# Kernel optimization log

Hardware: AMD Instinct MI355X
Metric: run time of the kernel (lower is better)

Reference implementation:

```python
import jax, jax.numpy as jnp
import numpy as np

N_NODES = 100000
N_EDGES = 1600000
N_FEAT = 64
HIDDEN = 64
N_GRAPHS = 256


def setup_inputs() -> dict:
    key = jax.random.key(0)
    ks = jax.random.split(key, 8)
    x = jax.random.normal(ks[0], (N_NODES, N_FEAT), dtype=jnp.float32)
    edge_index = jax.random.randint(ks[1], (2, N_EDGES), 0, N_NODES, dtype=jnp.int64)
    batch = jnp.sort(jax.random.randint(ks[2], (N_NODES,), 0, N_GRAPHS, dtype=jnp.int64))
    W1 = jax.random.normal(ks[3], (N_FEAT, HIDDEN), dtype=jnp.float32) / np.sqrt(N_FEAT)
    b1 = jnp.zeros((HIDDEN,), dtype=jnp.float32)
    W2 = jax.random.normal(ks[4], (HIDDEN, HIDDEN), dtype=jnp.float32) / np.sqrt(HIDDEN)
    b2 = jnp.zeros((HIDDEN,), dtype=jnp.float32)
    Wfc = jax.random.normal(ks[5], (HIDDEN, 1), dtype=jnp.float32) / np.sqrt(HIDDEN)
    bfc = jnp.zeros((1,), dtype=jnp.float32)
    return {"x": x, "edge_index": edge_index, "batch": batch,
            "W1": W1, "b1": b1, "W2": W2, "b2": b2, "Wfc": Wfc, "bfc": bfc}


def _gcn_conv(x, W, b, src, dst, norm, n_nodes):
    # h = X W, then symmetric-normalized scatter-add aggregation at dst
    h = x @ W  # [N, H]
    msg = h[src] * norm[:, None]  # [E+N, H] gather + scale
    agg = jax.ops.segment_sum(msg, dst, num_segments=n_nodes)
    return agg + b


def reference(x, edge_index, batch, W1, b1, W2, b2, Wfc, bfc):
    n = x.shape[0]
    loops = jnp.arange(n, dtype=edge_index.dtype)
    src = jnp.concatenate([edge_index[0], loops])  # add self-loops (GCNConv default)
    dst = jnp.concatenate([edge_index[1], loops])
    deg = jax.ops.segment_sum(jnp.ones_like(dst, dtype=x.dtype), dst, num_segments=n)
    dinv = jnp.where(deg > 0, jax.lax.rsqrt(deg), 0.0)
    norm = dinv[src] * dinv[dst]  # D^-1/2 (A+I) D^-1/2

    h = jax.nn.relu(_gcn_conv(x, W1, b1, src, dst, norm, n))  # dropout = identity (eval)
    h = jax.nn.relu(_gcn_conv(h, W2, b2, src, dst, norm, n))

    # global mean pool over graphs
    sums = jax.ops.segment_sum(h, batch, num_segments=N_GRAPHS)
    counts = jax.ops.segment_sum(jnp.ones((n,), dtype=h.dtype), batch, num_segments=N_GRAPHS)
    pooled = sums / jnp.maximum(counts, 1.0)[:, None]  # [G, H]
    return jax.nn.sigmoid(pooled @ Wfc + bfc)  # [G, 1]
```

## Files before the change

kernel.cpp:

```cpp
#include <hip/hip_runtime.h>
#include <hip/hip_fp16.h>
#include <math.h>

#define N_NODES  100000
#define N_EDGES  1600000
#define NF       64
#define N_GRAPHS 256

#define BSH   7
#define NB    ((N_NODES + 127) / 128)
#define BCAP  2600

typedef float f32x2 __attribute__((ext_vector_type(2)));

__global__ void k_zerocur(int* __restrict__ bucketCur, float* __restrict__ gsum,
                          int* __restrict__ Ah8, int* __restrict__ Ah8b) {
    int i = blockIdx.x * blockDim.x + threadIdx.x;
    if (i < NB) bucketCur[i] = 0;
    if (i < N_GRAPHS) gsum[i] = 0.0f;
    if (i < 16) {
        Ah8 [(size_t)N_NODES * 16 + i] = 0;
        Ah8b[(size_t)N_NODES * 16 + i] = 0;
    }
}

__global__ __launch_bounds__(1024) void k_bscatter(const int* __restrict__ src,
                                                   const int* __restrict__ dst,
                                                   int* __restrict__ bucketCur,
                                                   int* __restrict__ scratch) {
    __shared__ int hist[NB];
    __shared__ int bbase[NB];
    int t = threadIdx.x;
    for (int i = t; i < NB; i += 1024) hist[i] = 0;
    __syncthreads();
    int e0 = (blockIdx.x * 1024 + t) * 8;
    int d[8], s[8], r[8];
    bool act = (e0 + 7) < N_EDGES;
    if (act) {
        *(int4*)&d[0] = *(const int4*)(dst + e0);
        *(int4*)&d[4] = *(const int4*)(dst + e0 + 4);
        *(int4*)&s[0] = *(const int4*)(src + e0);
        *(int4*)&s[4] = *(const int4*)(src + e0 + 4);
#pragma unroll
        for (int k = 0; k < 8; ++k) r[k] = atomicAdd(&hist[d[k] >> BSH], 1);
    }
    __syncthreads();
    for (int i = t; i < NB; i += 1024)
        if (hist[i]) bbase[i] = atomicAdd(&bucketCur[i], hist[i]);
    __syncthreads();
    if (act) {
#pragma unroll
        for (int k = 0; k < 8; ++k) {
            int b = d[k] >> BSH;
            int pos = bbase[b] + r[k];
            if (pos < BCAP)
                scratch[b * BCAP + pos] = ((d[k] & 127) << 17) | s[k];
        }
    }
}

__global__ __launch_bounds__(1024) void k_bscan(const int* __restrict__ bucketCur,
                                                int* __restrict__ bucketPtr,
                                                int* __restrict__ rowptr) {
    int t = threadIdx.x;
    __shared__ int ps[1024];
    int v = (t < NB) ? min(bucketCur[t], BCAP) : 0;
    ps[t] = v;
    __syncthreads();
#pragma unroll
    for (int off = 1; off < 1024; off <<= 1) {
        int u = (t >= off) ? ps[t - off] : 0;
        __syncthreads();
        ps[t] += u;
        __syncthreads();
    }
    if (t < NB) bucketPtr[t] = ps[t] - v;
    if (t == NB - 1) {
        bucketPtr[NB] = ps[t];
        rowptr[N_NODES] = ps[t];
    }
}

__global__ __launch_bounds__(256) void k_bfinal(const int* __restrict__ bucketCur,
                                                const int* __restrict__ bucketPtr,
                                                const int* __restrict__ scratch,
                                                int* __restrict__ rowptr,
                                                float* __restrict__ dinv,
                                                int* __restrict__ col) {
    int b = blockIdx.x;
    int cnt  = min(bucketCur[b], BCAP);
    int base = bucketPtr[b];
    int node0 = b << BSH;
    __shared__ int hist[128];
    __shared__ int escan[128];
    __shared__ int ps[128];
    __shared__ int rnk[BCAP];
    int t = threadIdx.x;
    if (t < 128) hist[t] = 0;
    __syncthreads();
    const int* sp = scratch + b * BCAP;
    for (int j = t; j < cnt; j += 256)
        rnk[j] = atomicAdd(&hist[sp[j] >> 17], 1);
    __syncthreads();
    int hv = (t < 128) ? hist[t] : 0;
    if (t < 128) ps[t] = hv;
    __syncthreads();
#pragma unroll
    for (int off = 1; off < 128; off <<= 1) {
        int u = 0;
        if (t < 128 && t >= off) u = ps[t - off];
        __syncthreads();
        if (t < 128) ps[t] += u;
        __syncthreads();
    }
    if (t < 128) {
        int excl = ps[t] - hv;
        escan[t] = excl;
        int node = node0 + t;
        if (node < N_NODES) {
            rowptr[node] = base + excl;
            dinv[node] = rsqrtf((float)(hv + 1));
        }
    }
    __syncthreads();
    for (int j = t; j < cnt; j += 256) {
        int pk = sp[j];
        col[base + escan[pk >> 17] + rnk[j]] = pk & 0x1FFFF;
    }
}

__device__ __forceinline__ void agg8(const int* __restrict__ rowptr,
                                     const int* __restrict__ col,
                                     const int* __restrict__ Ah8,
                                     int n, int oct,
                                     f32x2& a0, f32x2& a1, f32x2& a2, f32x2& a3) {
    int nn  = (n < N_NODES) ? n : N_NODES;
    int beg = 0, cnt = 0;
    if (n < N_NODES) { beg = rowptr[n]; cnt = rowptr[n + 1] - beg; }
    const int* cp = col + beg;
    {
        int2 raw = *(const int2*)(Ah8 + (size_t)nn * 16 + oct * 2);
        a0 += __builtin_amdgcn_cvt_pk_f32_fp8(raw.x, false);
        a1 += __builtin_amdgcn_cvt_pk_f32_fp8(raw.x, true);
        a2 += __builtin_amdgcn_cvt_pk_f32_fp8(raw.y, false);
        a3 += __builtin_amdgcn_cvt_pk_f32_fp8(raw.y, true);
    }
    int c[8];
#pragma unroll
    for (int p = 0; p < 8; ++p) {
        int v = cp[p];
        c[p] = (p < cnt) ? v : N_NODES;
    }
    for (int base = 0; base < cnt; base += 8) {
        int2 rr[8];
#pragma unroll
        for (int p = 0; p < 8; ++p)
            rr[p] = *(const int2*)(Ah8 + (size_t)c[p] * 16 + oct * 2);
        int nb = base + 8;
#pragma unroll
        for (int p = 0; p < 8; ++p) {
            int v = cp[nb + p];
            c[p] = (nb + p < cnt) ? v : N_NODES;
        }
#pragma unroll
        for (int p = 0; p < 8; ++p) {
            a0 += __builtin_amdgcn_cvt_pk_f32_fp8(rr[p].x, false);
            a1 += __builtin_amdgcn_cvt_pk_f32_fp8(rr[p].x, true);
            a2 += __builtin_amdgcn_cvt_pk_f32_fp8(rr[p].y, false);
            a3 += __builtin_amdgcn_cvt_pk_f32_fp8(rr[p].y, true);
        }
    }
}

__global__ __launch_bounds__(256) void k_gemm(const float* __restrict__ X,
                                              const float* __restrict__ W,
                                              const float* __restrict__ dinv,
                                              int* __restrict__ Ah8) {
    __shared__ float Ws[64][64];
    __shared__ float Xs[64][68];
    int t  = threadIdx.x;
    int n0 = blockIdx.x * 64;

    for (int i = t; i < 64 * 64; i += 256) Ws[i >> 6][i & 63] = W[i];

#pragma unroll
    for (int p = 0; p < 4; ++p) {
        int flat = p * 256 + t;
        int nl = flat >> 4;
        int kg = flat & 15;
        int node = n0 + nl;
        float4 v = make_float4(0.f, 0.f, 0.f, 0.f);
        if (node < N_NODES)
            v = *(const float4*)(X + (size_t)node * NF + kg * 4);
        Xs[kg * 4 + 0][nl] = v.x;
        Xs[kg * 4 + 1][nl] = v.y;
        Xs[kg * 4 + 2][nl] = v.z;
        Xs[kg * 4 + 3][nl] = v.w;
    }
    __syncthreads();

    int tx = t & 15;
    int ty = t >> 4;
    float acc[4][4];
#pragma unroll
    for (int i = 0; i < 4; ++i)
#pragma unroll
        for (int j = 0; j < 4; ++j) acc[i][j] = 0.f;

#pragma unroll 8
    for (int k = 0; k < 64; ++k) {
        float4 wv = *(const float4*)&Ws[k][tx * 4];
        float4 xv = *(const float4*)&Xs[k][ty * 4];
        acc[0][0] += xv.x * wv.x; acc[0][1] += xv.x * wv.y;
        acc[0][2] += xv.x * wv.z; acc[0][3] += xv.x * wv.w;
        acc[1][0] += xv.y * wv.x; acc[1][1] += xv.y * wv.y;
        acc[1][2] += xv.y * wv.z; acc[1][3] += xv.y * wv.w;
        acc[2][0] += xv.z * wv.x; acc[2][1] += xv.z * wv.y;
        acc[2][2] += xv.z * wv.z; acc[2][3] += xv.z * wv.w;
        acc[3][0] += xv.w * wv.x; acc[3][1] += xv.w * wv.y;
        acc[3][2] += xv.w * wv.z; acc[3][3] += xv.w * wv.w;
    }

#pragma unroll
    for (int i = 0; i < 4; ++i) {
        int node = n0 + ty * 4 + i;
        if (node < N_NODES) {
            float dv = dinv[node];
            int pk = 0;
            pk = __builtin_amdgcn_cvt_pk_fp8_f32(acc[i][0] * dv, acc[i][1] * dv, pk, false);
            pk = __builtin_amdgcn_cvt_pk_fp8_f32(acc[i][2] * dv, acc[i][3] * dv, pk, true);
            Ah8[(size_t)node * 16 + tx] = pk;
        }
    }
}

__global__ __launch_bounds__(256) void k_pullgemm(const int* __restrict__ rowptr,
                                                  const int* __restrict__ col,
                                                  const float* __restrict__ dinv,
                                                  const int* __restrict__ Ah8,
                                                  const float* __restrict__ W,
                                                  const float* __restrict__ bias,
                                                  int* __restrict__ AhOut) {
    __shared__ float Ws[64][64];
    __shared__ float Xs[64][68];
    int t  = threadIdx.x;
    int n0 = blockIdx.x * 64;

    for (int i = t; i < 64 * 64; i += 256) Ws[i >> 6][i & 63] = W[i];

    int wv      = t >> 6;
    int lane    = t & 63;
    int nodeSub = lane >> 3;
    int oct     = lane & 7;

    float4 bA = *(const float4*)(bias + oct * 8);
    float4 bB = *(const float4*)(bias + oct * 8 + 4);

#pragma unroll
    for (int r = 0; r < 2; ++r) {
        int nl = wv * 16 + r * 8 + nodeSub;
        int n  = n0 + nl;
        f32x2 a0 = {0.f, 0.f}, a1 = {0.f, 0.f}, a2 = {0.f, 0.f}, a3 = {0.f, 0.f};
        agg8(rowptr, col, Ah8, n, oct, a0, a1, a2, a3);
        float dv = (n < N_NODES) ? dinv[n] : 0.f;
        float f0 = a0.x * dv + bA.x; Xs[oct * 8 + 0][nl] = f0 > 0.f ? f0 : 0.f;
        float f1 = a0.y * dv + bA.y; Xs[oct * 8 + 1][nl] = f1 > 0.f ? f1 : 0.f;
        float f2 = a1.x * dv + bA.z; Xs[oct * 8 + 2][nl] = f2 > 0.f ? f2 : 0.f;
        float f3 = a1.y * dv + bA.w; Xs[oct * 8 + 3][nl] = f3 > 0.f ? f3 : 0.f;
        float f4 = a2.x * dv + bB.x; Xs[oct * 8 + 4][nl] = f4 > 0.f ? f4 : 0.f;
        float f5 = a2.y * dv + bB.y; Xs[oct * 8 + 5][nl] = f5 > 0.f ? f5 : 0.f;
        float f6 = a3.x * dv + bB.z; Xs[oct * 8 + 6][nl] = f6 > 0.f ? f6 : 0.f;
        float f7 = a3.y * dv + bB.w; Xs[oct * 8 + 7][nl] = f7 > 0.f ? f7 : 0.f;
    }
    __syncthreads();

    int tx = t & 15;
    int ty = t >> 4;
    float acc[4][4];
#pragma unroll
    for (int i = 0; i < 4; ++i)
#pragma unroll
        for (int j = 0; j < 4; ++j) acc[i][j] = 0.f;

#pragma unroll 8
    for (int k = 0; k < 64; ++k) {
        float4 wvv = *(const float4*)&Ws[k][tx * 4];
        float4 xv  = *(const float4*)&Xs[k][ty * 4];
        acc[0][0] += xv.x * wvv.x; acc[0][1] += xv.x * wvv.y;
        acc[0][2] += xv.x * wvv.z; acc[0][3] += xv.x * wvv.w;
        acc[1][0] += xv.y * wvv.x; acc[1][1] += xv.y * wvv.y;
        acc[1][2] += xv.y * wvv.z; acc[1][3] += xv.y * wvv.w;
        acc[2][0] += xv.z * wvv.x; acc[2][1] += xv.z * wvv.y;
        acc[2][2] += xv.z * wvv.z; acc[2][3] += xv.z * wvv.w;
        acc[3][0] += xv.w * wvv.x; acc[3][1] += xv.w * wvv.y;
        acc[3][2] += xv.w * wvv.z; acc[3][3] += xv.w * wvv.w;
    }

#pragma unroll
    for (int i = 0; i < 4; ++i) {
        int node = n0 + ty * 4 + i;
        if (node < N_NODES) {
            float dv = dinv[node];
            int pk = 0;
            pk = __builtin_amdgcn_cvt_pk_fp8_f32(acc[i][0] * dv, acc[i][1] * dv, pk, false);
            pk = __builtin_amdgcn_cvt_pk_fp8_f32(acc[i][2] * dv, acc[i][3] * dv, pk, true);
            AhOut[(size_t)node * 16 + tx] = pk;
        }
    }
}

__global__ __launch_bounds__(256) void k_pullpool(const int* __restrict__ rowptr,
                                                  const int* __restrict__ col,
                                                  const float* __restrict__ dinv,
                                                  const int* __restrict__ Ah8,
                                                  const float* __restrict__ b2,
                                                  const float* __restrict__ Wfc,
                                                  const int* __restrict__ batch,
                                                  float* __restrict__ gsum) {
    int t       = threadIdx.x;
    int lane    = t & 63;
    int wv      = t >> 6;
    int nodeSub = lane >> 3;
    int oct     = lane & 7;
    int n = blockIdx.x * 32 + wv * 8 + nodeSub;

    float4 bA = *(const float4*)(b2 + oct * 8);
    float4 bB = *(const float4*)(b2 + oct * 8 + 4);
    float4 wA = *(const float4*)(Wfc + oct * 8);
    float4 wB = *(const float4*)(Wfc + oct * 8 + 4);

    f32x2 a0 = {0.f, 0.f}, a1 = {0.f, 0.f}, a2 = {0.f, 0.f}, a3 = {0.f, 0.f};
    agg8(rowptr, col, Ah8, n, oct, a0, a1, a2, a3);

    int   g  = (n < N_NODES) ? (int)batch[n] : -1;
    float dv = (n < N_NODES) ? dinv[n] : 0.f;

    float wsum = 0.f;
    float v;
    v = a0.x * dv + bA.x; wsum += (v > 0.f ? v : 0.f) * wA.x;
    v = a0.y * dv + bA.y; wsum += (v > 0.f ? v : 0.f) * wA.y;
    v = a1.x * dv + bA.z; wsum += (v > 0.f ? v : 0.f) * wA.z;
    v = a1.y * dv + bA.w; wsum += (v > 0.f ? v : 0.f) * wA.w;
    v = a2.x * dv + bB.x; wsum += (v > 0.f ? v : 0.f) * wB.x;
    v = a2.y * dv + bB.y; wsum += (v > 0.f ? v : 0.f) * wB.y;
    v = a3.x * dv + bB.z; wsum += (v > 0.f ? v : 0.f) * wB.z;
    v = a3.y * dv + bB.w; wsum += (v > 0.f ? v : 0.f) * wB.w;
    wsum += __shfl_xor(wsum, 1);
    wsum += __shfl_xor(wsum, 2);
    wsum += __shfl_xor(wsum, 4);

    float sv = (oct == 0) ? wsum : 0.f;
    int   gv = (oct == 0) ? g : -2;
#pragma unroll
    for (int off = 8; off < 64; off <<= 1) {
        float s2 = __shfl_down(sv, off);
        int   g2 = __shfl_down(gv, off);
        if (g2 == gv) sv += s2;
    }
    int gp = __shfl_up(gv, 8);
    bool head = (lane < 8) || (gp != gv);
    if (oct == 0 && g >= 0 && head) atomicAdd(&gsum[g], sv);
}

__device__ __forceinline__ int lower_bound_i(const int* __restrict__ a, int n, int key) {
    int lo = 0, hi = n;
    while (lo < hi) {
        int mid = (lo + hi) >> 1;
        if (a[mid] < key) lo = mid + 1; else hi = mid;
    }
    return lo;
}

__global__ void k_final(const int* __restrict__ batch,
                        const float* __restrict__ gsum,
                        const float* __restrict__ bfc,
                        float* __restrict__ out) {
    int g = blockIdx.x * blockDim.x + threadIdx.x;
    if (g < N_GRAPHS) {
        int lo = lower_bound_i(batch, N_NODES, g);
        int hi = lower_bound_i(batch, N_NODES, g + 1);
        float c = (hi > lo) ? (float)(hi - lo) : 1.0f;
        float v = gsum[g] / c + bfc[0];
        out[g] = 1.0f / (1.0f + expf(-v));
    }
}

extern "C" void kernel_launch(void* const* d_in, const int* in_sizes, int n_in,
                              void* d_out, int out_size, void* d_ws, size_t ws_size,
                              hipStream_t stream) {
    const float* x    = (const float*)d_in[0];
    const int*   ei   = (const int*)d_in[1];
    const int*   batch= (const int*)d_in[2];
    const float* W1   = (const float*)d_in[3];
    const float* b1   = (const float*)d_in[4];
    const float* W2   = (const float*)d_in[5];
    const float* b2   = (const float*)d_in[6];
    const float* Wfc  = (const float*)d_in[7];
    const float* bfc  = (const float*)d_in[8];
    float* out = (float*)d_out;

    const int* src = ei;
    const int* dst = ei + N_EDGES;

    int*    Ah8       = (int*)d_ws;
    int*    Ah8b      = Ah8 + (size_t)(N_NODES + 1) * 16;
    float*  dinv      = (float*)(Ah8b + (size_t)(N_NODES + 1) * 16);
    int*    rowptr    = (int*)(dinv + N_NODES);
    int*    bucketCur = rowptr + N_NODES + 1;
    int*    bucketPtr = bucketCur + NB;
    int*    col       = bucketPtr + NB + 1;
    float*  gsum      = (float*)(col + N_EDGES);
    int*    scratch   = (int*)(gsum + N_GRAPHS);

    const int BLK = 256;
    int g_gemm = (N_NODES + 63) / 64;
    int g_pp   = (N_NODES + 31) / 32;
    int g_bsc  = (N_EDGES / 8 + 1023) / 1024;

    k_zerocur<<<(NB + BLK - 1) / BLK, BLK, 0, stream>>>(bucketCur, gsum, Ah8, Ah8b);
    k_bscatter<<<g_bsc, 1024, 0, stream>>>(src, dst, bucketCur, scratch);
    k_bscan<<<1, 1024, 0, stream>>>(bucketCur, bucketPtr, rowptr);
    k_bfinal<<<NB, BLK, 0, stream>>>(bucketCur, bucketPtr, scratch, rowptr, dinv, col);

    k_gemm<<<g_gemm, BLK, 0, stream>>>(x, W1, dinv, Ah8);

    k_pullgemm<<<g_gemm, BLK, 0, stream>>>(rowptr, col, dinv, Ah8, W2, b1, Ah8b);

    k_pullpool<<<g_pp, BLK, 0, stream>>>(rowptr, col, dinv, Ah8b, b2, Wfc, batch, gsum);
    k_final<<<1, BLK, 0, stream>>>(batch, gsum, bfc, out);
}
```

Measured before the change: 236.5 us.

## Split CSR neighbor lists by source half and aggregate each half separately

During CSR construction, each destination's neighbor list is partitioned into sources below and above a fixed split, and a per-node rowmid pointer records the boundary. The aggregation kernels walk the low-half and high-half lists as two separate batched gather loops. The intent is to group gathers into one half of the feature table at a time for better cache locality. In exchange, each node pays two partially filled 8-wide batches instead of one, which adds padding loads and extra loop overhead.

```diff
diff --git a/kernel.cpp b/kernel.cpp
--- a/kernel.cpp
+++ b/kernel.cpp
@@ -6,6 +6,7 @@
 #define N_EDGES  1600000
 #define NF       64
 #define N_GRAPHS 256
+#define SRC_SPLIT 50000
 
 #define BSH   7
 #define NB    ((N_NODES + 127) / 128)
@@ -85,59 +86,91 @@
                                                 const int* __restrict__ bucketPtr,
                                                 const int* __restrict__ scratch,
                                                 int* __restrict__ rowptr,
+                                                int* __restrict__ rowmid,
                                                 float* __restrict__ dinv,
                                                 int* __restrict__ col) {
     int b = blockIdx.x;
     int cnt  = min(bucketCur[b], BCAP);
     int base = bucketPtr[b];
     int node0 = b << BSH;
-    __shared__ int hist[128];
-    __shared__ int escan[128];
-    __shared__ int ps[128];
+    __shared__ int hist[256];
+    __shared__ int escan[256];
+    __shared__ int ps[256];
     __shared__ int rnk[BCAP];
     int t = threadIdx.x;
-    if (t < 128) hist[t] = 0;
+    hist[t] = 0;
     __syncthreads();
     const int* sp = scratch + b * BCAP;
-    for (int j = t; j < cnt; j += 256)
-        rnk[j] = atomicAdd(&hist[sp[j] >> 17], 1);
-    __syncthreads();
-    int hv = (t < 128) ? hist[t] : 0;
-    if (t < 128) ps[t] = hv;
-    __syncthreads();
-#pragma unroll
-    for (int off = 1; off < 128; off <<= 1) {
-        int u = 0;
-        if (t < 128 && t >= off) u = ps[t - off];
+    for (int j = t; j < cnt; j += 256) {
+        int pk = sp[j];
+        int idx = ((pk >> 17) << 1) | ((pk & 0x1FFFF) >= SRC_SPLIT);
+        rnk[j] = atomicAdd(&hist[idx], 1);
+    }
+    __syncthreads();
+    int hv = hist[t];
+    ps[t] = hv;
+    __syncthreads();
+#pragma unroll
+    for (int off = 1; off < 256; off <<= 1) {
+        int u = (t >= off) ? ps[t - off] : 0;
         __syncthreads();
-        if (t < 128) ps[t] += u;
+        ps[t] += u;
         __syncthreads();
     }
+    escan[t] = ps[t] - hv;
+    __syncthreads();
     if (t < 128) {
-        int excl = ps[t] - hv;
-        escan[t] = excl;
         int node = node0 + t;
         if (node < N_NODES) {
-            rowptr[node] = base + excl;
-            dinv[node] = rsqrtf((float)(hv + 1));
-        }
-    }
-    __syncthreads();
+            int cL = hist[t * 2], cH = hist[t * 2 + 1];
+            rowptr[node] = base + escan[t * 2];
+            rowmid[node] = base + escan[t * 2 + 1];
+            dinv[node] = rsqrtf((float)(cL + cH + 1));
+        }
+    }
     for (int j = t; j < cnt; j += 256) {
         int pk = sp[j];
-        col[base + escan[pk >> 17] + rnk[j]] = pk & 0x1FFFF;
-    }
-}
-
-__device__ __forceinline__ void agg8(const int* __restrict__ rowptr,
+        int s = pk & 0x1FFFF;
+        int idx = ((pk >> 17) << 1) | (s >= SRC_SPLIT);
+        col[base + escan[idx] + rnk[j]] = s;
+    }
+}
+
+__device__ __forceinline__ void agg_half(const int* __restrict__ cp, int cnt,
+                                         const int* __restrict__ Ah8, int oct,
+                                         int c[8],
+                                         f32x2& a0, f32x2& a1, f32x2& a2, f32x2& a3) {
+    for (int base = 0; base < cnt; base += 8) {
+        int2 rr[8];
+#pragma unroll
+        for (int p = 0; p < 8; ++p)
+            rr[p] = *(const int2*)(Ah8 + (size_t)c[p] * 16 + oct * 2);
+        int nb = base + 8;
+#pragma unroll
+        for (int p = 0; p < 8; ++p) {
+            int v = cp[nb + p];
+            c[p] = (nb + p < cnt) ? v : N_NODES;
+        }
+#pragma unroll
+        for (int p = 0; p < 8; ++p) {
+            a0 += __builtin_amdgcn_cvt_pk_f32_fp8(rr[p].x, false);
+            a1 += __builtin_amdgcn_cvt_pk_f32_fp8(rr[p].x, true);
+            a2 += __builtin_amdgcn_cvt_pk_f32_fp8(rr[p].y, false);
+            a3 += __builtin_amdgcn_cvt_pk_f32_fp8(rr[p].y, true);
+        }
+    }
+}
+
+__device__ __forceinline__ void agg2(const int* __restrict__ rowptr,
+                                     const int* __restrict__ rowmid,
                                      const int* __restrict__ col,
                                      const int* __restrict__ Ah8,
                                      int n, int oct,
                                      f32x2& a0, f32x2& a1, f32x2& a2, f32x2& a3) {
     int nn  = (n < N_NODES) ? n : N_NODES;
-    int beg = 0, cnt = 0;
-    if (n < N_NODES) { beg = rowptr[n]; cnt = rowptr[n + 1] - beg; }
-    const int* cp = col + beg;
+    int beg = 0, mid = 0, end = 0;
+    if (n < N_NODES) { beg = rowptr[n]; mid = rowmid[n]; end = rowptr[n + 1]; }
+    int cntL = mid - beg, cntH = end - mid;
     {
         int2 raw = *(const int2*)(Ah8 + (size_t)nn * 16 + oct * 2);
         a0 += __builtin_amdgcn_cvt_pk_f32_fp8(raw.x, false);
@@ -145,31 +178,18 @@
         a2 += __builtin_amdgcn_cvt_pk_f32_fp8(raw.y, false);
         a3 += __builtin_amdgcn_cvt_pk_f32_fp8(raw.y, true);
     }
-    int c[8];
+    const int* cpL = col + beg;
+    const int* cpH = col + mid;
+    int cl[8], ch[8];
 #pragma unroll
     for (int p = 0; p < 8; ++p) {
-        int v = cp[p];
-        c[p] = (p < cnt) ? v : N_NODES;
-    }
-    for (int base = 0; base < cnt; base += 8) {
-        int2 rr[8];
-#pragma unroll
-        for (int p = 0; p < 8; ++p)
-            rr[p] = *(const int2*)(Ah8 + (size_t)c[p] * 16 + oct * 2);
-        int nb = base + 8;
-#pragma unroll
-        for (int p = 0; p < 8; ++p) {
-            int v = cp[nb + p];
-            c[p] = (nb + p < cnt) ? v : N_NODES;
-        }
-#pragma unroll
-        for (int p = 0; p < 8; ++p) {
-            a0 += __builtin_amdgcn_cvt_pk_f32_fp8(rr[p].x, false);
-            a1 += __builtin_amdgcn_cvt_pk_f32_fp8(rr[p].x, true);
-            a2 += __builtin_amdgcn_cvt_pk_f32_fp8(rr[p].y, false);
-            a3 += __builtin_amdgcn_cvt_pk_f32_fp8(rr[p].y, true);
-        }
-    }
+        int vl = cpL[p];
+        int vh = cpH[p];
+        cl[p] = (p < cntL) ? vl : N_NODES;
+        ch[p] = (p < cntH) ? vh : N_NODES;
+    }
+    agg_half(cpL, cntL, Ah8, oct, cl, a0, a1, a2, a3);
+    agg_half(cpH, cntH, Ah8, oct, ch, a0, a1, a2, a3);
 }
 
 __global__ __launch_bounds__(256) void k_gemm(const float* __restrict__ X,
@@ -235,6 +255,7 @@
 }
 
 __global__ __launch_bounds__(256) void k_pullgemm(const int* __restrict__ rowptr,
+                                                  const int* __restrict__ rowmid,
                                                   const int* __restrict__ col,
                                                   const float* __restrict__ dinv,
                                                   const int* __restrict__ Ah8,
@@ -261,7 +282,7 @@
         int nl = wv * 16 + r * 8 + nodeSub;
         int n  = n0 + nl;
         f32x2 a0 = {0.f, 0.f}, a1 = {0.f, 0.f}, a2 = {0.f, 0.f}, a3 = {0.f, 0.f};
-        agg8(rowptr, col, Ah8, n, oct, a0, a1, a2, a3);
+        agg2(rowptr, rowmid, col, Ah8, n, oct, a0, a1, a2, a3);
         float dv = (n < N_NODES) ? dinv[n] : 0.f;
         float f0 = a0.x * dv + bA.x; Xs[oct * 8 + 0][nl] = f0 > 0.f ? f0 : 0.f;
         float f1 = a0.y * dv + bA.y; Xs[oct * 8 + 1][nl] = f1 > 0.f ? f1 : 0.f;
@@ -310,6 +331,7 @@
 }
 
 __global__ __launch_bounds__(256) void k_pullpool(const int* __restrict__ rowptr,
+                                                  const int* __restrict__ rowmid,
                                                   const int* __restrict__ col,
                                                   const float* __restrict__ dinv,
                                                   const int* __restrict__ Ah8,
@@ -330,7 +352,7 @@
     float4 wB = *(const float4*)(Wfc + oct * 8 + 4);
 
     f32x2 a0 = {0.f, 0.f}, a1 = {0.f, 0.f}, a2 = {0.f, 0.f}, a3 = {0.f, 0.f};
-    agg8(rowptr, col, Ah8, n, oct, a0, a1, a2, a3);
+    agg2(rowptr, rowmid, col, Ah8, n, oct, a0, a1, a2, a3);
 
     int   g  = (n < N_NODES) ? (int)batch[n] : -1;
     float dv = (n < N_NODES) ? dinv[n] : 0.f;
@@ -406,7 +428,8 @@
     int*    Ah8b      = Ah8 + (size_t)(N_NODES + 1) * 16;
     float*  dinv      = (float*)(Ah8b + (size_t)(N_NODES + 1) * 16);
     int*    rowptr    = (int*)(dinv + N_NODES);
-    int*    bucketCur = rowptr + N_NODES + 1;
+    int*    rowmid    = rowptr + N_NODES + 1;
+    int*    bucketCur = rowmid + N_NODES;
     int*    bucketPtr = bucketCur + NB;
     int*    col       = bucketPtr + NB + 1;
     float*  gsum      = (float*)(col + N_EDGES);
@@ -420,12 +443,12 @@
     k_zerocur<<<(NB + BLK - 1) / BLK, BLK, 0, stream>>>(bucketCur, gsum, Ah8, Ah8b);
     k_bscatter<<<g_bsc, 1024, 0, stream>>>(src, dst, bucketCur, scratch);
     k_bscan<<<1, 1024, 0, stream>>>(bucketCur, bucketPtr, rowptr);
-    k_bfinal<<<NB, BLK, 0, stream>>>(bucketCur, bucketPtr, scratch, rowptr, dinv, col);
+    k_bfinal<<<NB, BLK, 0, stream>>>(bucketCur, bucketPtr, scratch, rowptr, rowmid, dinv, col);
 
     k_gemm<<<g_gemm, BLK, 0, stream>>>(x, W1, dinv, Ah8);
 
-    k_pullgemm<<<g_gemm, BLK, 0, stream>>>(rowptr, col, dinv, Ah8, W2, b1, Ah8b);
-
-    k_pullpool<<<g_pp, BLK, 0, stream>>>(rowptr, col, dinv, Ah8b, b2, Wfc, batch, gsum);
+    k_pullgemm<<<g_gemm, BLK, 0, stream>>>(rowptr, rowmid, col, dinv, Ah8, W2, b1, Ah8b);
+
+    k_pullpool<<<g_pp, BLK, 0, stream>>>(rowptr, rowmid, col, dinv, Ah8b, b2, Wfc, batch, gsum);
     k_final<<<1, BLK, 0, stream>>>(batch, gsum, bfc, out);
 }
```

Result: no change. 238.3 us (+0.8%).
